# Kernel tuning notes

Hardware: AMD Instinct MI355X
Metric: run time of the kernel (lower is better)

Reference implementation:

```python
import jax, jax.numpy as jnp
import numpy as np

N_NODES = 50000
N_EDGES = 600000
D = 128
REL_DIM = 100
N_REL = 40
NEG_SLOPE = 0.2


def setup_inputs() -> dict:
    key = jax.random.key(0)
    ks = jax.random.split(key, 9)
    return {
        "node_features": jax.random.normal(ks[0], (N_NODES, D), jnp.float32),
        "edge_index": jax.random.randint(ks[1], (2, N_EDGES), 0, N_NODES, jnp.int64 if jax.config.jax_enable_x64 else jnp.int32),
        "edge_type": jax.random.randint(ks[2], (N_EDGES,), 0, N_REL, jnp.int32),
        "W": jax.random.normal(ks[3], (D, D), jnp.float32) * (1.0 / np.sqrt(D)),
        "W_r": jax.random.normal(ks[4], (REL_DIM, D), jnp.float32) * (1.0 / np.sqrt(REL_DIM)),
        "a": jax.random.normal(ks[5], (3 * D,), jnp.float32) * (1.0 / np.sqrt(3 * D)),
        "W_res": jax.random.normal(ks[6], (D, D), jnp.float32) * (1.0 / np.sqrt(D)),
        "b_res": jax.random.normal(ks[7], (D,), jnp.float32) * 0.01,
        "rel_emb": jax.random.normal(ks[8], (N_REL, REL_DIM), jnp.float32),
    }


def _segment_softmax(logits, seg_ids, num_segments):
    # numerically stable softmax over edges grouped by destination node
    seg_max = jax.ops.segment_max(logits, seg_ids, num_segments=num_segments)
    seg_max = jnp.where(jnp.isfinite(seg_max), seg_max, 0.0)
    e = jnp.exp(logits - seg_max[seg_ids])
    seg_sum = jax.ops.segment_sum(e, seg_ids, num_segments=num_segments)
    return e / (seg_sum[seg_ids] + 1e-16)


def reference(node_features, edge_index, edge_type, W, W_r, a, W_res, b_res, rel_emb):
    src = edge_index[0]  # x_j (source / message sender)
    dst = edge_index[1]  # x_i (target / aggregation index)

    h = node_features @ W                      # [N, D]
    h_rel = rel_emb[edge_type] @ W_r           # [E, D]
    h_src = h[src]                             # [E, D]
    h_dst = h[dst]                             # [E, D]

    # attention logit per edge: a . cat(W x_i, W x_j, W_r r_e), LeakyReLU(0.2)
    logit = h_dst @ a[:D] + h_src @ a[D:2 * D] + h_rel @ a[2 * D:]  # [E]
    logit = jax.nn.leaky_relu(logit, NEG_SLOPE)

    alpha = _segment_softmax(logit, dst, N_NODES)  # [E]

    agg = jax.ops.segment_sum(h_src * alpha[:, None], dst, num_segments=N_NODES)  # [N, D]

    out = agg + node_features @ W_res + b_res  # residual connection
    # LayerG: SELU then dropout (identity in eval mode)
    return jax.nn.selu(out)
```

## Files before the change

### kernel.cpp

```cpp
#include <hip/hip_runtime.h>
#include <hip/hip_bf16.h>

typedef __attribute__((ext_vector_type(8))) short bf16x8;
typedef __attribute__((ext_vector_type(4))) float f32x4;

#define LDS_STRIDE 528
#define CAP 64

__device__ __forceinline__ unsigned short f2bf(float f) {
    union { float f; unsigned int u; } v; v.f = f;
    unsigned int r = (v.u + 0x7FFF + ((v.u >> 16) & 1)) >> 16;
    return (unsigned short)r;
}
__device__ __forceinline__ float bf2f(unsigned int hbits) {
    union { unsigned int u; float f; } v; v.u = hbits << 16;
    return v.f;
}

__global__ __launch_bounds__(256) void setup_kernel(
    int* __restrict__ counts, int N,
    const float* __restrict__ W, const float* __restrict__ W_res,
    unsigned short* __restrict__ WbPack,
    const float* __restrict__ W_r, const float* __restrict__ a,
    const float* __restrict__ rel_emb, float* __restrict__ rl,
    int n_rel, int rel_dim, int zb)
{
    __shared__ float a3[128];
    __shared__ float wa[128];
    int bid = blockIdx.x;
    int tid = threadIdx.x;
    if (bid < zb) {
        int i = bid * 256 + tid;
        if (i < N) counts[i] = 0;
        return;
    }
    if (bid < zb + 16) {
        int g = (bid - zb) * 256 + tid;
        int t = g >> 8;
        int s = (g >> 6) & 3;
        int lane = g & 63;
        int ncol = ((t & 7) << 4) + (lane & 15);
        int k0 = s * 32 + ((lane >> 4) << 3);
        const float* srcw = (t < 8) ? W : W_res;
        unsigned short* dst = WbPack + ((size_t)(t * 4 + s) * 64 + lane) * 8;
        #pragma unroll
        for (int j = 0; j < 8; ++j) dst[j] = f2bf(srcw[(size_t)(k0 + j) * 128 + ncol]);
        return;
    }
    if (tid < 128) {
        a3[tid] = a[256 + tid];
    }
    __syncthreads();
    if (tid < rel_dim) {
        float s = 0.f;
        for (int d = 0; d < 128; ++d) s += W_r[tid * 128 + d] * a3[d];
        wa[tid] = s;
    }
    __syncthreads();
    if (tid < n_rel) {
        float s = 0.f;
        for (int k = 0; k < rel_dim; ++k) s += rel_emb[tid * rel_dim + k] * wa[k];
        rl[tid] = s;
    }
}

__global__ __launch_bounds__(256) void gemm_dual_kernel(
    const float* __restrict__ X, const unsigned short* __restrict__ WbPack,
    const float* __restrict__ b_res, const float* __restrict__ a,
    unsigned short* __restrict__ hb, unsigned short* __restrict__ resb,
    float* __restrict__ p, float* __restrict__ q, int M)
{
    __shared__ __align__(16) unsigned char smem[64 * LDS_STRIDE];
    __shared__ float pq_s[128];
    const int tid = threadIdx.x;
    const int lane = tid & 63;
    const int wave = tid >> 6;
    const int rowbase = blockIdx.x * 64;
    const int c16 = lane & 15;
    const int kq = lane >> 4;

    if (tid < 128) pq_s[tid] = 0.f;

    bf16x8 wfrag[4][4];
    #pragma unroll
    for (int tt = 0; tt < 4; ++tt)
        #pragma unroll
        for (int s = 0; s < 4; ++s)
            wfrag[tt][s] = *(const bf16x8*)(WbPack + ((size_t)((wave * 4 + tt) * 4 + s) * 64 + lane) * 8);

    float bres[4];
    #pragma unroll
    for (int tt = 0; tt < 4; ++tt) {
        int t = wave * 4 + tt;
        bres[tt] = (t >= 8) ? b_res[(t - 8) * 16 + c16] : 0.f;
    }
    float pa[4], qa[4];
    #pragma unroll
    for (int tt = 0; tt < 4; ++tt) {
        int col = (wave * 4 + tt) * 16 + c16;
        pa[tt] = (wave < 2) ? a[col] : 0.f;
        qa[tt] = (wave < 2) ? a[128 + col] : 0.f;
    }

    #pragma unroll
    for (int j = 0; j < 8; ++j) {
        int ch = j * 256 + tid;
        int r = ch >> 5;
        int c = ch & 31;
        int gr = rowbase + r; if (gr >= M) gr = M - 1;
        float4 v = *(const float4*)(X + (size_t)gr * 128 + c * 4);
        unsigned int u0 = ((unsigned)f2bf(v.y) << 16) | f2bf(v.x);
        unsigned int u1 = ((unsigned)f2bf(v.w) << 16) | f2bf(v.z);
        *(uint2*)(smem + r * LDS_STRIDE + c * 8) = make_uint2(u0, u1);
    }
    __syncthreads();

    f32x4 acc[4][4];
    #pragma unroll
    for (int rt = 0; rt < 4; ++rt)
        #pragma unroll
        for (int tt = 0; tt < 4; ++tt) acc[rt][tt] = (f32x4){0.f, 0.f, 0.f, 0.f};

    #pragma unroll
    for (int s = 0; s < 4; ++s) {
        #pragma unroll
        for (int rt = 0; rt < 4; ++rt) {
            int row = rt * 16 + c16;
            bf16x8 af = *(const bf16x8*)(smem + row * LDS_STRIDE + s * 64 + kq * 16);
            #pragma unroll
            for (int tt = 0; tt < 4; ++tt)
                acc[rt][tt] = __builtin_amdgcn_mfma_f32_16x16x32_bf16(af, wfrag[tt][s], acc[rt][tt], 0, 0, 0);
        }
    }
    __syncthreads();

    if (wave < 2) {
        #pragma unroll
        for (int rt = 0; rt < 4; ++rt) {
            #pragma unroll
            for (int i = 0; i < 4; ++i) {
                float pp = 0.f, qq = 0.f;
                #pragma unroll
                for (int tt = 0; tt < 4; ++tt) {
                    pp += acc[rt][tt][i] * pa[tt];
                    qq += acc[rt][tt][i] * qa[tt];
                }
                #pragma unroll
                for (int d = 1; d < 16; d <<= 1) {
                    pp += __shfl_xor(pp, d, 64);
                    qq += __shfl_xor(qq, d, 64);
                }
                if (c16 == 0) {
                    int r = rt * 16 + kq * 4 + i;
                    atomicAdd(&pq_s[r], pp);
                    atomicAdd(&pq_s[64 + r], qq);
                }
            }
        }
    }

    #pragma unroll
    for (int rt = 0; rt < 4; ++rt) {
        #pragma unroll
        for (int tt = 0; tt < 4; ++tt) {
            int colall = (wave * 4 + tt) * 16 + c16;
            #pragma unroll
            for (int i = 0; i < 4; ++i) {
                int row = rt * 16 + kq * 4 + i;
                *(unsigned short*)(smem + row * LDS_STRIDE + colall * 2) = f2bf(acc[rt][tt][i] + bres[tt]);
            }
        }
    }
    __syncthreads();

    #pragma unroll
    for (int j = 0; j < 4; ++j) {
        int ch = j * 256 + tid;
        int r = ch >> 4;
        int c = ch & 15;
        int gr = rowbase + r;
        uint4 hv = *(const uint4*)(smem + r * LDS_STRIDE + c * 16);
        uint4 rv = *(const uint4*)(smem + r * LDS_STRIDE + 256 + c * 16);
        if (gr < M) {
            *(uint4*)(hb + (size_t)gr * 128 + c * 8) = hv;
            *(uint4*)(resb + (size_t)gr * 128 + c * 8) = rv;
        }
    }
    if (tid < 64) {
        int gr = rowbase + tid;
        if (gr < M) { p[gr] = pq_s[tid]; q[gr] = pq_s[64 + tid]; }
    }
}

__global__ __launch_bounds__(256) void edge_kernel(
    const int* __restrict__ src, const int* __restrict__ dst, const int* __restrict__ etype,
    int* __restrict__ counts, unsigned int* __restrict__ slots, int E)
{
    const int xcd = blockIdx.x & 7;
    const int stripe = blockIdx.x >> 3;
    const int base = stripe * 2048 + threadIdx.x;
    #pragma unroll
    for (int k = 0; k < 8; ++k) {
        int e = base + k * 256;
        if (e < E) {
            int d = dst[e];
            if (((d >> 2) & 7) == xcd) {
                int s = src[e];
                int t = etype[e];
                int rk = atomicAdd(&counts[d], 1);
                if (rk < CAP)
                    slots[(size_t)d * CAP + rk] = (unsigned int)s | ((unsigned int)t << 16);
            }
        }
    }
}

__global__ __launch_bounds__(256) void agg_kernel(
    const unsigned short* __restrict__ hb, const unsigned short* __restrict__ resb,
    const float* __restrict__ p, const float* __restrict__ q, const float* __restrict__ rl,
    const int* __restrict__ counts, const unsigned int* __restrict__ slots,
    float* __restrict__ out, int N, int n_rel)
{
    __shared__ float rls[64];
    if (threadIdx.x < n_rel) rls[threadIdx.x] = rl[threadIdx.x];
    __syncthreads();

    const int tid = threadIdx.x;
    const int lane = tid & 63;
    const int sub = lane & 31;
    const int shbase = lane & 32;
    int node = blockIdx.x * 8 + ((tid >> 6) << 1) + (lane >> 5);
    if (node >= N) return;
    int nn = min(counts[node], CAP);

    float pnode = p[node];
    float a0 = 0.f, a1 = 0.f, a2 = 0.f, a3 = 0.f;
    float ssum = 0.f;
    const unsigned short* hsub = hb + sub * 4;

    for (int c = 0; c < nn; c += 32) {
        int m = min(32, nn - c);
        float se = 0.f;
        int sv = 0;
        if (sub < m) {
            unsigned int pk = slots[(size_t)node * CAP + c + sub];
            sv = (int)(pk & 0xffffu);
            int t = (int)(pk >> 16);
            float l = pnode + q[sv] + rls[t];
            l = (l > 0.f) ? l : 0.2f * l;
            se = __expf(l);
        }
        ssum += se;

        int j = 0;
        for (; j + 7 < m; j += 8) {
            float w[8]; int r[8]; uint2 v[8];
            #pragma unroll
            for (int u = 0; u < 8; ++u) { w[u] = __shfl(se, shbase + j + u); r[u] = __shfl(sv, shbase + j + u); }
            #pragma unroll
            for (int u = 0; u < 8; ++u) v[u] = *(const uint2*)(hsub + (size_t)r[u] * 128);
            #pragma unroll
            for (int u = 0; u < 8; ++u) {
                a0 += w[u] * bf2f(v[u].x & 0xffff);
                a1 += w[u] * bf2f(v[u].x >> 16);
                a2 += w[u] * bf2f(v[u].y & 0xffff);
                a3 += w[u] * bf2f(v[u].y >> 16);
            }
        }
        for (; j + 3 < m; j += 4) {
            float w[4]; int r[4]; uint2 v[4];
            #pragma unroll
            for (int u = 0; u < 4; ++u) { w[u] = __shfl(se, shbase + j + u); r[u] = __shfl(sv, shbase + j + u); }
            #pragma unroll
            for (int u = 0; u < 4; ++u) v[u] = *(const uint2*)(hsub + (size_t)r[u] * 128);
            #pragma unroll
            for (int u = 0; u < 4; ++u) {
                a0 += w[u] * bf2f(v[u].x & 0xffff);
                a1 += w[u] * bf2f(v[u].x >> 16);
                a2 += w[u] * bf2f(v[u].y & 0xffff);
                a3 += w[u] * bf2f(v[u].y >> 16);
            }
        }
        for (; j < m; ++j) {
            float w = __shfl(se, shbase + j);
            int r = __shfl(sv, shbase + j);
            uint2 v = *(const uint2*)(hsub + (size_t)r * 128);
            a0 += w * bf2f(v.x & 0xffff);
            a1 += w * bf2f(v.x >> 16);
            a2 += w * bf2f(v.y & 0xffff);
            a3 += w * bf2f(v.y >> 16);
        }
    }

    #pragma unroll
    for (int d = 1; d < 32; d <<= 1) ssum += __shfl_xor(ssum, d, 64);
    float inv = 1.0f / (ssum + 1e-16f);
    a0 *= inv; a1 *= inv; a2 *= inv; a3 *= inv;

    uint2 rv = *(const uint2*)(resb + (size_t)node * 128 + sub * 4);
    float o0 = a0 + bf2f(rv.x & 0xffff), o1 = a1 + bf2f(rv.x >> 16);
    float o2 = a2 + bf2f(rv.y & 0xffff), o3 = a3 + bf2f(rv.y >> 16);
    const float SC = 1.0507009873554805f, AL = 1.6732632423543772f;
    o0 = (o0 > 0.f) ? SC * o0 : SC * AL * (__expf(o0) - 1.f);
    o1 = (o1 > 0.f) ? SC * o1 : SC * AL * (__expf(o1) - 1.f);
    o2 = (o2 > 0.f) ? SC * o2 : SC * AL * (__expf(o2) - 1.f);
    o3 = (o3 > 0.f) ? SC * o3 : SC * AL * (__expf(o3) - 1.f);
    f32x4 ov = (f32x4){o0, o1, o2, o3};
    __builtin_nontemporal_store(ov, (f32x4*)(out + (size_t)node * 128 + sub * 4));
}

extern "C" void kernel_launch(void* const* d_in, const int* in_sizes, int n_in,
                              void* d_out, int out_size, void* d_ws, size_t ws_size,
                              hipStream_t stream)
{
    const float* X      = (const float*)d_in[0];
    const int*   ei     = (const int*)d_in[1];
    const int*   etype  = (const int*)d_in[2];
    const float* W      = (const float*)d_in[3];
    const float* W_r    = (const float*)d_in[4];
    const float* a      = (const float*)d_in[5];
    const float* W_res  = (const float*)d_in[6];
    const float* b_res  = (const float*)d_in[7];
    const float* rel_emb= (const float*)d_in[8];

    const int N = in_sizes[0] / 128;
    const int E = in_sizes[2];
    const int n_rel = in_sizes[8] / 100;
    const int* src = ei;
    const int* dst = ei + E;

    char* w = (char*)d_ws;
    auto alloc = [&](size_t bytes) -> void* {
        void* ptr = (void*)w;
        w += (bytes + 255) & ~(size_t)255;
        return ptr;
    };
    unsigned short* WbPack = (unsigned short*)alloc((size_t)16 * 4 * 64 * 8 * 2);
    unsigned short* hb     = (unsigned short*)alloc((size_t)N * 128 * 2);
    unsigned short* resb   = (unsigned short*)alloc((size_t)N * 128 * 2);
    float* p       = (float*)alloc((size_t)N * 4);
    float* q       = (float*)alloc((size_t)N * 4);
    float* rl      = (float*)alloc(64 * 4);
    int*   counts  = (int*)alloc((size_t)N * 4);
    unsigned int* slots = (unsigned int*)alloc((size_t)N * CAP * 4);
    float* out     = (float*)d_out;

    const int zb = (N + 255) / 256;
    const int gemm_blocks = (N + 63) / 64;
    const int agg_blocks = (N + 7) / 8;
    const int stripes = (E + 2047) / 2048;
    const int edge_blocks = stripes * 8;

    setup_kernel<<<zb + 17, 256, 0, stream>>>(counts, N, W, W_res, WbPack,
                                              W_r, a, rel_emb, rl, n_rel, 100, zb);
    gemm_dual_kernel<<<gemm_blocks, 256, 0, stream>>>(X, WbPack, b_res, a, hb, resb, p, q, N);
    edge_kernel<<<edge_blocks, 256, 0, stream>>>(src, dst, etype, counts, slots, E);
    agg_kernel<<<agg_blocks, 256, 0, stream>>>(hb, resb, p, q, rl, counts, slots, out, N, n_rel);
}
```

Baseline: 178.9 us.

## Fuse edge bucketing into GEMM kernel via interleaved block roles

Merges the edge-bucketing kernel into the dual GEMM kernel. Odd-numbered blocks in the first range handle 2048 edges each and the rest compute GEMM tiles, so the atomic-heavy scatter overlaps with the compute-bound GEMM and one launch is removed. It also drops the XCD-partitioned striping, where each edge was read by 8 blocks and filtered by destination. Each edge is now read once with nontemporal loads, at the cost of losing the L2 locality the XCD filtering gave the atomics on counts. Edge blocks still allocate the large GEMM shared-memory buffer, which may reduce occupancy for them.

```diff
diff --git a/kernel.cpp b/kernel.cpp
--- a/kernel.cpp
+++ b/kernel.cpp
@@ -64,18 +64,41 @@
     }
 }
 
-__global__ __launch_bounds__(256) void gemm_dual_kernel(
+__global__ __launch_bounds__(256) void gemm_edge_kernel(
     const float* __restrict__ X, const unsigned short* __restrict__ WbPack,
     const float* __restrict__ b_res, const float* __restrict__ a,
     unsigned short* __restrict__ hb, unsigned short* __restrict__ resb,
-    float* __restrict__ p, float* __restrict__ q, int M)
+    float* __restrict__ p, float* __restrict__ q, int M,
+    const int* __restrict__ src, const int* __restrict__ dst_i, const int* __restrict__ etype,
+    int* __restrict__ counts, unsigned int* __restrict__ slots, int E, int EB)
 {
     __shared__ __align__(16) unsigned char smem[64 * LDS_STRIDE];
     __shared__ float pq_s[128];
     const int tid = threadIdx.x;
+    const int bid = blockIdx.x;
+
+    const bool is_edge = (bid < 2 * EB) && (bid & 1);
+    if (is_edge) {
+        const int base = (bid >> 1) * 2048 + tid;
+        #pragma unroll
+        for (int k = 0; k < 8; ++k) {
+            int e = base + k * 256;
+            if (e < E) {
+                int d = __builtin_nontemporal_load(dst_i + e);
+                int s = __builtin_nontemporal_load(src + e);
+                int t = __builtin_nontemporal_load(etype + e);
+                int rk = atomicAdd(&counts[d], 1);
+                if (rk < CAP)
+                    slots[(size_t)d * CAP + rk] = (unsigned int)s | ((unsigned int)t << 16);
+            }
+        }
+        return;
+    }
+    const int gid = (bid < 2 * EB) ? (bid >> 1) : (bid - EB);
+
     const int lane = tid & 63;
     const int wave = tid >> 6;
-    const int rowbase = blockIdx.x * 64;
+    const int rowbase = gid * 64;
     const int c16 = lane & 15;
     const int kq = lane >> 4;
 
@@ -192,29 +215,6 @@
     }
 }
 
-__global__ __launch_bounds__(256) void edge_kernel(
-    const int* __restrict__ src, const int* __restrict__ dst, const int* __restrict__ etype,
-    int* __restrict__ counts, unsigned int* __restrict__ slots, int E)
-{
-    const int xcd = blockIdx.x & 7;
-    const int stripe = blockIdx.x >> 3;
-    const int base = stripe * 2048 + threadIdx.x;
-    #pragma unroll
-    for (int k = 0; k < 8; ++k) {
-        int e = base + k * 256;
-        if (e < E) {
-            int d = dst[e];
-            if (((d >> 2) & 7) == xcd) {
-                int s = src[e];
-                int t = etype[e];
-                int rk = atomicAdd(&counts[d], 1);
-                if (rk < CAP)
-                    slots[(size_t)d * CAP + rk] = (unsigned int)s | ((unsigned int)t << 16);
-            }
-        }
-    }
-}
-
 __global__ __launch_bounds__(256) void agg_kernel(
     const unsigned short* __restrict__ hb, const unsigned short* __restrict__ resb,
     const float* __restrict__ p, const float* __restrict__ q, const float* __restrict__ rl,
@@ -348,12 +348,12 @@
     const int zb = (N + 255) / 256;
     const int gemm_blocks = (N + 63) / 64;
     const int agg_blocks = (N + 7) / 8;
-    const int stripes = (E + 2047) / 2048;
-    const int edge_blocks = stripes * 8;
+    const int edge_blocks = (E + 2047) / 2048;
+    const int fused_blocks = gemm_blocks + edge_blocks;
 
     setup_kernel<<<zb + 17, 256, 0, stream>>>(counts, N, W, W_res, WbPack,
                                               W_r, a, rel_emb, rl, n_rel, 100, zb);
-    gemm_dual_kernel<<<gemm_blocks, 256, 0, stream>>>(X, WbPack, b_res, a, hb, resb, p, q, N);
-    edge_kernel<<<edge_blocks, 256, 0, stream>>>(src, dst, etype, counts, slots, E);
+    gemm_edge_kernel<<<fused_blocks, 256, 0, stream>>>(X, WbPack, b_res, a, hb, resb, p, q, N,
+                                                       src, dst, etype, counts, slots, E, edge_blocks);
     agg_kernel<<<agg_blocks, 256, 0, stream>>>(hb, resb, p, q, rl, counts, slots, out, N, n_rel);
 }
```

Result: faster. 173.6 us (-3.0%).
